# Optimization experiments

Hardware: AMD Instinct MI355X
Metric: run time of the kernel (lower is better)

The kernel has to match this reference:

```python
import jax, jax.numpy as jnp
import numpy as np

HD = 256          # hidden_dim[0]
KF = 2            # k factor
KD = HD * KF      # 512, bilinear feature dim
L = 2000          # hard-coded sequence length
B = 4
NEG = np.float32(np.finfo(np.float32).min)  # finite min, NOT -inf (matches torch code)
EPS = 1e-5


def _fc(x, V, g, b):
    # weight_norm(Linear, dim=None): W = g * V / ||V||_F, then ReLU
    W = (g / jnp.linalg.norm(V)) * V  # [KD, HD]
    return jax.nn.relu(jnp.einsum('blh,kh->blk', x, W) + b)


def setup_inputs() -> dict:
    key = jax.random.key(0)
    ks = jax.random.split(key, 12)
    X = jax.random.normal(ks[0], (B, L, HD), dtype=jnp.float32)
    Y = jax.random.normal(ks[1], (B, L, HD), dtype=jnp.float32)
    mask1 = jax.random.bernoulli(ks[2], 0.8, (B, L)).astype(jnp.float32)
    mask2 = jax.random.bernoulli(ks[3], 0.8, (B, L)).astype(jnp.float32)
    # Q_net / K_net params (single weight-normed linear each)
    Qv = jax.random.normal(ks[4], (KD, HD), dtype=jnp.float32) * 0.05
    Qg = jnp.asarray(1.0, dtype=jnp.float32)
    Qb = jax.random.normal(ks[5], (KD,), dtype=jnp.float32) * 0.05
    Kv = jax.random.normal(ks[6], (KD, HD), dtype=jnp.float32) * 0.05
    Kg = jnp.asarray(1.0, dtype=jnp.float32)
    Kb = jax.random.normal(ks[7], (KD,), dtype=jnp.float32) * 0.05
    h_mat = jax.random.normal(ks[8], (KD,), dtype=jnp.float32)   # (1,1,KD) squeezed
    h_bias = jax.random.normal(ks[9], (), dtype=jnp.float32)     # (1,1,1) squeezed
    gamma = jnp.ones((KD,), dtype=jnp.float32)                   # BatchNorm1d affine
    beta = jnp.zeros((KD,), dtype=jnp.float32)
    return {"X": X, "Y": Y, "mask1": mask1, "mask2": mask2,
            "Qv": Qv, "Qg": Qg, "Qb": Qb, "Kv": Kv, "Kg": Kg, "Kb": Kb,
            "h_mat": h_mat, "h_bias": h_bias, "gamma": gamma, "beta": beta}


def _masked_softmax(A, m_row):
    # m_row: [B,1,L], broadcasts over axis 1; softmax over dim 1 as in torch
    logits = jnp.where(m_row > 0, A, NEG)
    att = jax.nn.softmax(logits, axis=1)
    return m_row * att


def reference(X, Y, mask1, mask2, Qv, Qg, Qb, Kv, Kg, Kb, h_mat, h_bias, gamma, beta):
    A1_X = _fc(X, Qv, Qg, Qb)  # [B,L,KD]
    A1_Y = _fc(Y, Kv, Kg, Kb)
    A2_Y = _fc(Y, Qv, Qg, Qb)
    A2_X = _fc(X, Kv, Kg, Kb)
    # bilinear co-attention maps [B,L,L]
    A1 = jnp.einsum('bvk,bqk->bvq', A1_X * h_mat, A1_Y) + h_bias
    A2 = jnp.einsum('bqk,bvk->bqv', A2_Y * h_mat, A2_X) + h_bias
    m1r = mask1[:, None, :]  # mask1_attend[b,v,q] = mask1[b,q]
    m2r = mask2[:, None, :]
    alpha = _masked_softmax(A1, m2r)
    logits_X = jnp.einsum('bvq,bqk->bvk', alpha, A1_Y) * mask1[:, :, None]
    beta_att = _masked_softmax(A2, m1r)
    logits_Y = jnp.einsum('bqv,bvk->bqk', beta_att, A2_X) * mask2[:, :, None]
    # AvgPool2d((2000,1)) == mean over sequence dim
    pooled = logits_X.mean(axis=1) + logits_Y.mean(axis=1)  # [B,KD]
    # BatchNorm1d training-mode forward (biased batch stats)
    mu = pooled.mean(axis=0)
    var = pooled.var(axis=0)
    return gamma * (pooled - mu) * jax.lax.rsqrt(var + EPS) + beta
```

## Files before the change

kernel.cpp:

```cpp
#include <hip/hip_runtime.h>

#define NB 4
#define LSEQ 2000
#define HD 256
#define KD 512
#define LPAD 2048
#define SMALL_N 18562

using short8 = __attribute__((ext_vector_type(8))) short;
using f32x4  = __attribute__((ext_vector_type(4))) float;
typedef unsigned short u16;

__device__ __forceinline__ float b2f(u16 u) { return __uint_as_float(((unsigned)u) << 16); }
__device__ __forceinline__ u16 f2b(float f) {
    unsigned u = __float_as_uint(f);
    u += 0x7FFFu + ((u >> 16) & 1u);
    return (u16)(u >> 16);
}
__device__ __forceinline__ bool detect32(const void* gamma) {
    return ((const float*)gamma)[0] == 1.0f;
}
__device__ __forceinline__ void gl_lds16(const u16* g, short* l) {
    __builtin_amdgcn_global_load_lds(
        (const __attribute__((address_space(1))) unsigned int*)g,
        (__attribute__((address_space(3))) unsigned int*)l, 16, 0, 0);
}

__global__ void convert_kernel(const void* X, const void* Y, const void* Qv, const void* Kv,
                               const void* m1, const void* m2, const void* Qb, const void* Kb,
                               const void* hm, const void* Qg, const void* Kg,
                               const void* gamma, const void* beta,
                               u16* __restrict__ Xb, u16* __restrict__ Yb,
                               u16* __restrict__ Qvb, u16* __restrict__ Kvb,
                               float* __restrict__ smallf, float* __restrict__ ssqp,
                               float* __restrict__ pooled)
{
    const bool is32 = detect32(gamma);
    const int seg = blockIdx.y;
    if (seg < 4) {
        const void* src = seg == 0 ? X : seg == 1 ? Y : seg == 2 ? Qv : Kv;
        u16* dst = seg == 0 ? Xb : seg == 1 ? Yb : seg == 2 ? Qvb : Kvb;
        const int n = (seg < 2) ? NB * LSEQ * HD : KD * HD;
        const int i0 = (blockIdx.x * 256 + threadIdx.x) * 8;
        if (i0 >= n) return;
        uint4 pack;
        u16* v = (u16*)&pack;
        if (is32) {
            float4 fa = ((const float4*)src)[(i0 >> 2)];
            float4 fb = ((const float4*)src)[(i0 >> 2) + 1];
            v[0] = f2b(fa.x); v[1] = f2b(fa.y); v[2] = f2b(fa.z); v[3] = f2b(fa.w);
            v[4] = f2b(fb.x); v[5] = f2b(fb.y); v[6] = f2b(fb.z); v[7] = f2b(fb.w);
        } else {
            pack = ((const uint4*)src)[i0 >> 3];
        }
        ((uint4*)dst)[i0 >> 3] = pack;
        if (seg >= 2) {
            float s = 0.f;
            #pragma unroll
            for (int j = 0; j < 8; ++j) { float f = b2f(v[j]); s = fmaf(f, f, s); }
            #pragma unroll
            for (int off = 32; off > 0; off >>= 1) s += __shfl_xor(s, off);
            __shared__ float red[4];
            if ((threadIdx.x & 63) == 0) red[threadIdx.x >> 6] = s;
            __syncthreads();
            if (threadIdx.x == 0)
                ssqp[(seg - 2) * 64 + blockIdx.x] = red[0] + red[1] + red[2] + red[3];
        }
    } else {
        const int i0 = (blockIdx.x * 256 + threadIdx.x) * 4;
        #pragma unroll
        for (int j = 0; j < 4; ++j)
            if (i0 + j < NB * KD) pooled[i0 + j] = 0.f;
        for (int i = i0; i < i0 + 4; ++i) {
            if (i >= SMALL_N) break;
            const void* src; int off;
            if      (i <  8000) { src = m1;    off = i; }
            else if (i < 16000) { src = m2;    off = i - 8000; }
            else if (i < 16512) { src = Qb;    off = i - 16000; }
            else if (i < 17024) { src = Kb;    off = i - 16512; }
            else if (i < 17536) { src = hm;    off = i - 17024; }
            else if (i < 18048) { src = gamma; off = i - 17536; }
            else if (i < 18560) { src = beta;  off = i - 18048; }
            else if (i == 18560) {
                float f = ((const float*)Qg)[0];
                smallf[i] = (f == 1.0f) ? 1.0f : b2f(((const u16*)Qg)[0]);
                continue;
            } else {
                float f = ((const float*)Kg)[0];
                smallf[i] = (f == 1.0f) ? 1.0f : b2f(((const u16*)Kg)[0]);
                continue;
            }
            smallf[i] = is32 ? ((const float*)src)[off] : b2f(((const u16*)src)[off]);
        }
    }
}

__global__ __launch_bounds__(256, 2)
void fc_kernel(const u16* __restrict__ X, const u16* __restrict__ Y,
               const u16* __restrict__ Qv, const u16* __restrict__ Kv,
               const float* __restrict__ Qbf, const float* __restrict__ Kbf,
               const float* __restrict__ hf, const float* __restrict__ gv,
               const float* __restrict__ ssqp, u16* __restrict__ fc)
{
    const int id = blockIdx.x;
    const int z7 = id & 7, idx = id >> 3;
    const int t = z7 + 8 * (idx & 1);
    const int tile = idx >> 1;
    const int mt = tile & 15, nt = tile >> 4;
    const int b = t >> 2, which = t & 3;
    const u16* In = ((which == 0) | (which == 3)) ? (X + (size_t)b * LSEQ * HD)
                                                  : (Y + (size_t)b * LSEQ * HD);
    const bool isQ = (which == 0) | (which == 2);
    const u16* W      = isQ ? Qv : Kv;
    const float* bias = isQ ? Qbf : Kbf;
    const int j = isQ ? 0 : 1;
    float ssq = 0.f;
    for (int i = 0; i < 64; ++i) ssq += ssqp[j * 64 + i];
    const float s = gv[j] / sqrtf(ssq);
    u16* out = fc + (size_t)t * LSEQ * KD;

    __shared__ __align__(16) short As[2][128 * 32];
    __shared__ __align__(16) short Bs[2][128 * 32];

    const int tid = threadIdx.x;
    const int lane = tid & 63, wave = tid >> 6;
    const int wm = wave >> 1, wn = wave & 1;
    const int quad = lane >> 4, l15 = lane & 15;
    const int sr = tid >> 2, sc = tid & 3;
    const int scz = sc ^ ((sr >> 1) & 3);
    const int m0 = mt * 128, n0 = nt * 128;

    int gm0 = min(m0 + sr, LSEQ - 1), gm1 = min(m0 + sr + 64, LSEQ - 1);
    const u16* pA0 = In + (size_t)gm0 * HD + scz * 8;
    const u16* pA1 = In + (size_t)gm1 * HD + scz * 8;
    const u16* pB0 = W + (size_t)(n0 + sr) * HD + scz * 8;
    const u16* pB1 = W + (size_t)(n0 + sr + 64) * HD + scz * 8;
    const int dof = sr * 32 + sc * 8;

    int aoff[4], boff[4];
    #pragma unroll
    for (int i = 0; i < 4; ++i) {
        int ra = wm * 64 + i * 16 + l15;
        aoff[i] = ra * 32 + (quad ^ ((ra >> 1) & 3)) * 8;
        int rb = wn * 64 + i * 16 + l15;
        boff[i] = rb * 32 + (quad ^ ((rb >> 1) & 3)) * 8;
    }

    gl_lds16(pA0, &As[0][dof]);
    gl_lds16(pA1, &As[0][64 * 32 + dof]);
    gl_lds16(pB0, &Bs[0][dof]);
    gl_lds16(pB1, &Bs[0][64 * 32 + dof]);
    __syncthreads();

    f32x4 acc[4][4] = {};

    for (int kt = 0; kt < 8; ++kt) {
        const int cur = kt & 1, nxt = cur ^ 1;
        if (kt < 7) {
            const int ko = (kt + 1) * 32;
            gl_lds16(pA0 + ko, &As[nxt][dof]);
            gl_lds16(pA1 + ko, &As[nxt][64 * 32 + dof]);
            gl_lds16(pB0 + ko, &Bs[nxt][dof]);
            gl_lds16(pB1 + ko, &Bs[nxt][64 * 32 + dof]);
        }
        short8 af[4], bf[4];
        #pragma unroll
        for (int i = 0; i < 4; ++i) af[i] = *(const short8*)&As[cur][aoff[i]];
        #pragma unroll
        for (int i = 0; i < 4; ++i) bf[i] = *(const short8*)&Bs[cur][boff[i]];
        #pragma unroll
        for (int mi = 0; mi < 4; ++mi)
            #pragma unroll
            for (int ni = 0; ni < 4; ++ni)
                acc[mi][ni] = __builtin_amdgcn_mfma_f32_16x16x32_bf16(af[mi], bf[ni], acc[mi][ni], 0, 0, 0);
        __syncthreads();
    }

    #pragma unroll
    for (int ni = 0; ni < 4; ++ni) {
        int n = n0 + wn * 64 + ni * 16 + l15;
        float bv = bias[n];
        float hv = isQ ? hf[n] : 1.0f;
        #pragma unroll
        for (int mi = 0; mi < 4; ++mi) {
            int mb = m0 + wm * 64 + mi * 16 + quad * 4;
            #pragma unroll
            for (int r = 0; r < 4; ++r) {
                int m = mb + r;
                if (m < LSEQ) {
                    float v = fmaf(s, acc[mi][ni][r], bv);
                    v = v > 0.f ? v : 0.f;
                    out[(size_t)m * KD + n] = f2b(v * hv);
                }
            }
        }
    }
}

__global__ __launch_bounds__(512, 2)
void colsm_kernel(const u16* __restrict__ fc, const float* __restrict__ m1f,
                  const float* __restrict__ m2f,
                  float* __restrict__ part_d, float* __restrict__ part_n)
{
    const int id = blockIdx.x;
    const int z = id & 7, rem = id >> 3;
    const int vs = rem & 15, qt = rem >> 4;
    const int a = z >> 2, b = z & 3;
    const u16* R  = fc + (size_t)(b * 4 + (a == 0 ? 1 : 3)) * LSEQ * KD;
    const u16* Sm = fc + (size_t)(b * 4 + (a == 0 ? 0 : 2)) * LSEQ * KD;
    const float* wmask = (a == 0 ? m1f : m2f) + (size_t)b * LSEQ;

    __shared__ __align__(16) short Rs[2][256 * 32];
    __shared__ __align__(16) short Ss[2][128 * 32];
    __shared__ float ldsD[256][2];
    __shared__ float ldsN[256][2];

    const int tid = threadIdx.x;
    const int lane = tid & 63, wave = tid >> 6;
    const int wm = wave >> 1, wn = wave & 1;
    const int quad = lane >> 4, l15 = lane & 15;
    const int sr = tid >> 2, sc = tid & 3;
    const int scz = sc ^ ((sr >> 1) & 3);
    const int r0 = qt * 256, c0 = vs * 128;

    int gr0 = min(r0 + sr, LSEQ - 1), gr1 = min(r0 + sr + 128, LSEQ - 1);
    int gc0 = min(c0 + sr, LSEQ - 1);
    const u16* pR0 = R  + (size_t)gr0 * KD + scz * 8;
    const u16* pR1 = R  + (size_t)gr1 * KD + scz * 8;
    const u16* pS0 = Sm + (size_t)gc0 * KD + scz * 8;
    const int dof = sr * 32 + sc * 8;

    int aoff[4], boff[4];
    #pragma unroll
    for (int i = 0; i < 4; ++i) {
        int ra = wm * 64 + i * 16 + l15;
        aoff[i] = ra * 32 + (quad ^ ((ra >> 1) & 3)) * 8;
        int rb = wn * 64 + i * 16 + l15;
        boff[i] = rb * 32 + (quad ^ ((rb >> 1) & 3)) * 8;
    }

    gl_lds16(pR0, &Rs[0][dof]);
    gl_lds16(pR1, &Rs[0][128 * 32 + dof]);
    gl_lds16(pS0, &Ss[0][dof]);
    __syncthreads();

    f32x4 acc[4][4] = {};

    for (int kt = 0; kt < 16; ++kt) {
        const int cur = kt & 1, nxt = cur ^ 1;
        if (kt < 15) {
            const int ko = (kt + 1) * 32;
            gl_lds16(pR0 + ko, &Rs[nxt][dof]);
            gl_lds16(pR1 + ko, &Rs[nxt][128 * 32 + dof]);
            gl_lds16(pS0 + ko, &Ss[nxt][dof]);
        }
        short8 af[4], bf[4];
        #pragma unroll
        for (int i = 0; i < 4; ++i) af[i] = *(const short8*)&Rs[cur][aoff[i]];
        #pragma unroll
        for (int i = 0; i < 4; ++i) bf[i] = *(const short8*)&Ss[cur][boff[i]];
        #pragma unroll
        for (int mi = 0; mi < 4; ++mi)
            #pragma unroll
            for (int ni = 0; ni < 4; ++ni)
                acc[mi][ni] = __builtin_amdgcn_mfma_f32_16x16x32_bf16(af[mi], bf[ni], acc[mi][ni], 0, 0, 0);
        __syncthreads();
    }

    float wv[4], vv[4];
    #pragma unroll
    for (int ni = 0; ni < 4; ++ni) {
        int cg = c0 + wn * 64 + ni * 16 + l15;
        bool valid = cg < LSEQ;
        vv[ni] = valid ? 1.f : 0.f;
        wv[ni] = valid ? wmask[cg] : 0.f;
    }
    #pragma unroll
    for (int mi = 0; mi < 4; ++mi)
        #pragma unroll
        for (int r = 0; r < 4; ++r) {
            float d = 0.f, n = 0.f;
            #pragma unroll
            for (int ni = 0; ni < 4; ++ni) {
                float e = __expf(acc[mi][ni][r]);
                d = fmaf(vv[ni], e, d);
                n = fmaf(wv[ni], e, n);
            }
            #pragma unroll
            for (int off = 1; off < 16; off <<= 1) {
                d += __shfl_xor(d, off);
                n += __shfl_xor(n, off);
            }
            if (l15 == 0) {
                int row = wm * 64 + mi * 16 + quad * 4 + r;
                ldsD[row][wn] = d;
                ldsN[row][wn] = n;
            }
        }
    __syncthreads();
    if (tid < 256) {
        int q = r0 + tid;
        if (q < LSEQ) {
            size_t p = ((size_t)(z * 16 + vs)) * LPAD + q;
            part_d[p] = ldsD[tid][0] + ldsD[tid][1];
            part_n[p] = ldsN[tid][0] + ldsN[tid][1];
        }
    }
}

__global__ void pooledc_kernel(const u16* __restrict__ fc,
                               const float* __restrict__ part_d, const float* __restrict__ part_n,
                               const float* __restrict__ m1f, const float* __restrict__ m2f,
                               float* __restrict__ pooled)
{
    const int b = blockIdx.x, rs = blockIdx.y;
    const int tid = threadIdx.x;
    __shared__ float c1s[100], c2s[100];

    if (tid < 100) {
        int r = rs * 100 + tid;
        float d1 = 0.f, n1 = 0.f, d2 = 0.f, n2 = 0.f;
        #pragma unroll
        for (int vs = 0; vs < 16; ++vs) {
            size_t p1 = ((size_t)(b * 16 + vs)) * LPAD + r;
            size_t p2 = ((size_t)((4 + b) * 16 + vs)) * LPAD + r;
            d1 += part_d[p1]; n1 += part_n[p1];
            d2 += part_d[p2]; n2 += part_n[p2];
        }
        c1s[tid] = m2f[b * LSEQ + r] * n1 / d1;
        c2s[tid] = m1f[b * LSEQ + r] * n2 / d2;
    }
    __syncthreads();

    const int k8 = (tid & 63) * 8;
    const int rg = tid >> 6;
    const u16* YK = fc + (size_t)(b * 4 + 1) * LSEQ * KD;
    const u16* XK = fc + (size_t)(b * 4 + 3) * LSEQ * KD;
    float s[8] = {};
    const int lbeg = rg * 25, lend = lbeg + 25;
    for (int lr = lbeg; lr < lend; ++lr) {
        int r = rs * 100 + lr;
        float w1 = c1s[lr], w2 = c2s[lr];
        uint4 uy = *(const uint4*)(YK + (size_t)r * KD + k8);
        uint4 ux = *(const uint4*)(XK + (size_t)r * KD + k8);
        const u16* py = (const u16*)&uy;
        const u16* px = (const u16*)&ux;
        #pragma unroll
        for (int j = 0; j < 8; ++j)
            s[j] = fmaf(w1, b2f(py[j]), fmaf(w2, b2f(px[j]), s[j]));
    }
    #pragma unroll
    for (int j = 0; j < 8; ++j)
        atomicAdd(&pooled[b * KD + k8 + j], s[j] * (1.0f / LSEQ));
}

__global__ void ln_kernel(const float* __restrict__ pooled, const float* __restrict__ gammaf,
                          const float* __restrict__ betaf, const void* __restrict__ gamma_orig,
                          void* __restrict__ out)
{
    int k = blockIdx.x * 256 + threadIdx.x;
    float p[NB];
    #pragma unroll
    for (int b = 0; b < NB; ++b) p[b] = pooled[b * KD + k];
    float mu = 0.25f * (p[0] + p[1] + p[2] + p[3]);
    float var = 0.f;
    #pragma unroll
    for (int b = 0; b < NB; ++b) { float d = p[b] - mu; var = fmaf(d, d, var); }
    var *= 0.25f;
    float inv = rsqrtf(var + 1e-5f);
    float g = gammaf[k], be = betaf[k];
    const bool is32 = detect32(gamma_orig);
    #pragma unroll
    for (int b = 0; b < NB; ++b) {
        float v = fmaf(g * (p[b] - mu), inv, be);
        if (is32) ((float*)out)[b * KD + k] = v;
        else      ((u16*)out)[b * KD + k] = f2b(v);
    }
}

extern "C" void kernel_launch(void* const* d_in, const int* in_sizes, int n_in,
                              void* d_out, int out_size, void* d_ws, size_t ws_size,
                              hipStream_t stream)
{
    const void* X  = d_in[0];
    const void* Y  = d_in[1];
    const void* m1 = d_in[2];
    const void* m2 = d_in[3];
    const void* Qv = d_in[4];
    const void* Qg = d_in[5];
    const void* Qb = d_in[6];
    const void* Kv = d_in[7];
    const void* Kg = d_in[8];
    const void* Kb = d_in[9];
    const void* h  = d_in[10];
    const void* gamma = d_in[12];
    const void* beta  = d_in[13];

    char* ws = (char*)d_ws;
    size_t off = 0;
    u16* Xb  = (u16*)(ws + off); off += (size_t)NB * LSEQ * HD * 2;
    u16* Yb  = (u16*)(ws + off); off += (size_t)NB * LSEQ * HD * 2;
    u16* Qvb = (u16*)(ws + off); off += (size_t)KD * HD * 2;
    u16* Kvb = (u16*)(ws + off); off += (size_t)KD * HD * 2;
    float* smallf = (float*)(ws + off); off += ((size_t)SMALL_N * 4 + 15) / 16 * 16;
    float* ssqp   = (float*)(ws + off); off += 128 * 4;
    u16* fc  = (u16*)(ws + off); off += (size_t)16 * LSEQ * KD * 2;
    float* part_d = (float*)(ws + off); off += (size_t)8 * 16 * LPAD * 4;
    float* part_n = (float*)(ws + off); off += (size_t)8 * 16 * LPAD * 4;
    float* pooled = (float*)(ws + off); off += (size_t)NB * KD * 4;

    const float* m1f = smallf;
    const float* m2f = smallf + 8000;
    const float* Qbf = smallf + 16000;
    const float* Kbf = smallf + 16512;
    const float* hf  = smallf + 17024;
    const float* gmf = smallf + 17536;
    const float* bef = smallf + 18048;
    const float* gv  = smallf + 18560;

    convert_kernel<<<dim3(1000, 5), 256, 0, stream>>>(X, Y, Qv, Kv, m1, m2, Qb, Kb, h, Qg, Kg,
                                                      gamma, beta, Xb, Yb, Qvb, Kvb,
                                                      smallf, ssqp, pooled);
    fc_kernel     <<<1024, 256, 0, stream>>>(Xb, Yb, Qvb, Kvb, Qbf, Kbf, hf, gv, ssqp, fc);
    colsm_kernel  <<<1024, 512, 0, stream>>>(fc, m1f, m2f, part_d, part_n);
    pooledc_kernel<<<dim3(4, 20), 256, 0, stream>>>(fc, part_d, part_n, m1f, m2f, pooled);
    ln_kernel     <<<2, 256, 0, stream>>>(pooled, gmf, bef, gamma, d_out);
}
```

Measured before the change: 203.6 us.

## Triple-buffer LDS loads with one barrier per k-step in GEMM kernels

Both the fc and colsm GEMM loops move from double to triple buffering. Each k-step now uses explicit vmcnt waits and a single s_barrier, and loads run two stages ahead instead of one, which removes the trailing __syncthreads. The colsm reduction scratch now reuses the Rs buffer so that LDS does not grow by a separate array, and the fc block-to-task mapping is reordered so that concurrently scheduled blocks share batch inputs. The added LDS per block may reduce occupancy, and the hand-written waitcnt counts depend on how the compiler emits the loads.

```diff
diff --git a/kernel.cpp b/kernel.cpp
--- a/kernel.cpp
+++ b/kernel.cpp
@@ -104,10 +104,11 @@
 {
     const int id = blockIdx.x;
     const int z7 = id & 7, idx = id >> 3;
-    const int t = z7 + 8 * (idx & 1);
+    const int b = z7 & 3, w = (z7 >> 2) * 2 + (idx & 1);
+    const int t = 4 * b + w;
     const int tile = idx >> 1;
     const int mt = tile & 15, nt = tile >> 4;
-    const int b = t >> 2, which = t & 3;
+    const int which = t & 3;
     const u16* In = ((which == 0) | (which == 3)) ? (X + (size_t)b * LSEQ * HD)
                                                   : (Y + (size_t)b * LSEQ * HD);
     const bool isQ = (which == 0) | (which == 2);
@@ -119,8 +120,8 @@
     const float s = gv[j] / sqrtf(ssq);
     u16* out = fc + (size_t)t * LSEQ * KD;
 
-    __shared__ __align__(16) short As[2][128 * 32];
-    __shared__ __align__(16) short Bs[2][128 * 32];
+    __shared__ __align__(16) short As[3][128 * 32];
+    __shared__ __align__(16) short Bs[3][128 * 32];
 
     const int tid = threadIdx.x;
     const int lane = tid & 63, wave = tid >> 6;
@@ -146,34 +147,34 @@
         boff[i] = rb * 32 + (quad ^ ((rb >> 1) & 3)) * 8;
     }
 
-    gl_lds16(pA0, &As[0][dof]);
-    gl_lds16(pA1, &As[0][64 * 32 + dof]);
-    gl_lds16(pB0, &Bs[0][dof]);
-    gl_lds16(pB1, &Bs[0][64 * 32 + dof]);
-    __syncthreads();
+    auto stage = [&](int buf, int ko) {
+        gl_lds16(pA0 + ko, &As[buf][dof]);
+        gl_lds16(pA1 + ko, &As[buf][64 * 32 + dof]);
+        gl_lds16(pB0 + ko, &Bs[buf][dof]);
+        gl_lds16(pB1 + ko, &Bs[buf][64 * 32 + dof]);
+    };
+    stage(0, 0);
+    stage(1, 32);
 
     f32x4 acc[4][4] = {};
 
+    #pragma unroll
     for (int kt = 0; kt < 8; ++kt) {
-        const int cur = kt & 1, nxt = cur ^ 1;
-        if (kt < 7) {
-            const int ko = (kt + 1) * 32;
-            gl_lds16(pA0 + ko, &As[nxt][dof]);
-            gl_lds16(pA1 + ko, &As[nxt][64 * 32 + dof]);
-            gl_lds16(pB0 + ko, &Bs[nxt][dof]);
-            gl_lds16(pB1 + ko, &Bs[nxt][64 * 32 + dof]);
-        }
+        const int cur = kt % 3;
+        if (kt == 7) asm volatile("s_waitcnt vmcnt(0)" ::: "memory");
+        else         asm volatile("s_waitcnt vmcnt(4)" ::: "memory");
+        asm volatile("s_barrier" ::: "memory");
         short8 af[4], bf[4];
         #pragma unroll
         for (int i = 0; i < 4; ++i) af[i] = *(const short8*)&As[cur][aoff[i]];
         #pragma unroll
         for (int i = 0; i < 4; ++i) bf[i] = *(const short8*)&Bs[cur][boff[i]];
+        if (kt + 2 < 8) stage((kt + 2) % 3, (kt + 2) * 32);
         #pragma unroll
         for (int mi = 0; mi < 4; ++mi)
             #pragma unroll
             for (int ni = 0; ni < 4; ++ni)
                 acc[mi][ni] = __builtin_amdgcn_mfma_f32_16x16x32_bf16(af[mi], bf[ni], acc[mi][ni], 0, 0, 0);
-        __syncthreads();
     }
 
     #pragma unroll
@@ -210,10 +211,8 @@
     const u16* Sm = fc + (size_t)(b * 4 + (a == 0 ? 0 : 2)) * LSEQ * KD;
     const float* wmask = (a == 0 ? m1f : m2f) + (size_t)b * LSEQ;
 
-    __shared__ __align__(16) short Rs[2][256 * 32];
-    __shared__ __align__(16) short Ss[2][128 * 32];
-    __shared__ float ldsD[256][2];
-    __shared__ float ldsN[256][2];
+    __shared__ __align__(16) short Rs[3][256 * 32];
+    __shared__ __align__(16) short Ss[3][128 * 32];
 
     const int tid = threadIdx.x;
     const int lane = tid & 63, wave = tid >> 6;
@@ -239,33 +238,37 @@
         boff[i] = rb * 32 + (quad ^ ((rb >> 1) & 3)) * 8;
     }
 
-    gl_lds16(pR0, &Rs[0][dof]);
-    gl_lds16(pR1, &Rs[0][128 * 32 + dof]);
-    gl_lds16(pS0, &Ss[0][dof]);
-    __syncthreads();
+    auto stage = [&](int buf, int ko) {
+        gl_lds16(pR0 + ko, &Rs[buf][dof]);
+        gl_lds16(pR1 + ko, &Rs[buf][128 * 32 + dof]);
+        gl_lds16(pS0 + ko, &Ss[buf][dof]);
+    };
+    stage(0, 0);
+    stage(1, 32);
 
     f32x4 acc[4][4] = {};
 
+    #pragma unroll
     for (int kt = 0; kt < 16; ++kt) {
-        const int cur = kt & 1, nxt = cur ^ 1;
-        if (kt < 15) {
-            const int ko = (kt + 1) * 32;
-            gl_lds16(pR0 + ko, &Rs[nxt][dof]);
-            gl_lds16(pR1 + ko, &Rs[nxt][128 * 32 + dof]);
-            gl_lds16(pS0 + ko, &Ss[nxt][dof]);
-        }
+        const int cur = kt % 3;
+        if (kt == 15) asm volatile("s_waitcnt vmcnt(0)" ::: "memory");
+        else          asm volatile("s_waitcnt vmcnt(3)" ::: "memory");
+        asm volatile("s_barrier" ::: "memory");
         short8 af[4], bf[4];
         #pragma unroll
         for (int i = 0; i < 4; ++i) af[i] = *(const short8*)&Rs[cur][aoff[i]];
         #pragma unroll
         for (int i = 0; i < 4; ++i) bf[i] = *(const short8*)&Ss[cur][boff[i]];
+        if (kt + 2 < 16) stage((kt + 2) % 3, (kt + 2) * 32);
         #pragma unroll
         for (int mi = 0; mi < 4; ++mi)
             #pragma unroll
             for (int ni = 0; ni < 4; ++ni)
                 acc[mi][ni] = __builtin_amdgcn_mfma_f32_16x16x32_bf16(af[mi], bf[ni], acc[mi][ni], 0, 0, 0);
-        __syncthreads();
-    }
+    }
+    __syncthreads();
+    float* ldsD = (float*)&Rs[0][0];
+    float* ldsN = ldsD + 512;
 
     float wv[4], vv[4];
     #pragma unroll
@@ -293,8 +296,8 @@
             }
             if (l15 == 0) {
                 int row = wm * 64 + mi * 16 + quad * 4 + r;
-                ldsD[row][wn] = d;
-                ldsN[row][wn] = n;
+                ldsD[row * 2 + wn] = d;
+                ldsN[row * 2 + wn] = n;
             }
         }
     __syncthreads();
@@ -302,8 +305,8 @@
         int q = r0 + tid;
         if (q < LSEQ) {
             size_t p = ((size_t)(z * 16 + vs)) * LPAD + q;
-            part_d[p] = ldsD[tid][0] + ldsD[tid][1];
-            part_n[p] = ldsN[tid][0] + ldsN[tid][1];
+            part_d[p] = ldsD[tid * 2] + ldsD[tid * 2 + 1];
+            part_n[p] = ldsN[tid * 2] + ldsN[tid * 2 + 1];
         }
     }
 }
```

New measurement: 204.9 us. No clear change (+0.6%).
